# Kernel optimization log

Hardware: AMD Instinct MI355X
Metric: run time of the kernel (lower is better)

Reference implementation:

```python
import jax, jax.numpy as jnp
import numpy as np

EMD_DIM = 64
NB_EMD = 512


def setup_inputs() -> dict:
    key = jax.random.key(0)
    k_x, k_e = jax.random.split(key)
    x = jax.random.normal(k_x, (32, 64, 64, EMD_DIM), dtype=jnp.float32)
    # codebook buffer, shape [emd_dim, nb_emd] as in the torch module
    embed = jax.random.normal(k_e, (EMD_DIM, NB_EMD), dtype=jnp.float32)
    return {"x": x, "embed": embed}


def reference(x, embed):
    # Eval-mode forward (the EMA buffer update only runs under self.training
    # and does not affect this forward's outputs).
    flatten = x.reshape(-1, EMD_DIM)                      # [N, d]
    dist = (jnp.sum(flatten * flatten, axis=1, keepdims=True)
            - 2.0 * flatten @ embed
            + jnp.sum(embed * embed, axis=0, keepdims=True))  # [N, K]
    emd_id_flat = jnp.argmax(-dist, axis=1)               # nearest code index [N]
    emd_id = emd_id_flat.reshape(x.shape[:-1])            # [B, H, W]
    q = jnp.take(embed.T, emd_id, axis=0)                 # gather codes -> [B,H,W,d]
    diff = jnp.mean((jax.lax.stop_gradient(q) - x) ** 2)  # commitment loss
    q_st = x + jax.lax.stop_gradient(q - x)               # straight-through
    return (q_st, diff, emd_id)
```

## Files before the change

kernel.cpp:

```cpp
#include <hip/hip_runtime.h>

#define N_VEC 131072
#define D 64
#define K 512
#define GUARD 0.05f
#define NB_GATHER 2048
#define FB_Q 16

typedef __attribute__((ext_vector_type(8))) short bf16x8;
typedef __attribute__((ext_vector_type(4))) float f32x4;

static __device__ __forceinline__ short f2bf(float f) {
  unsigned u = __builtin_bit_cast(unsigned, f);
  u += 0x7fffu + ((u >> 16) & 1u);
  return (short)(u >> 16);
}
static __device__ __forceinline__ float bf2f(short h) {
  unsigned u = ((unsigned)(unsigned short)h) << 16;
  return __builtin_bit_cast(float, u);
}
static __device__ __forceinline__ void split8(const float4 f0, const float4 f1,
                                              bf16x8& h, bf16x8& m) {
  const float v[8] = {f0.x, f0.y, f0.z, f0.w, f1.x, f1.y, f1.z, f1.w};
#pragma unroll
  for (int j = 0; j < 8; ++j) {
    const short hh = f2bf(v[j]);
    h[j] = hh;
    m[j] = f2bf(v[j] - bf2f(hh));
  }
}

__global__ __launch_bounds__(64) void vq_prep_kernel(
    const float* __restrict__ embed, float* __restrict__ et,
    float* __restrict__ nrm, bf16x8* __restrict__ F, int* __restrict__ cnt)
{
  const int b = blockIdx.x;
  const int lane = threadIdx.x;
  if (b < 32) {
    const int row = lane & 15;
    const int kg  = lane >> 4;
    const int code = b * 16 + row;
#pragma unroll
    for (int c = 0; c < 2; ++c) {
      bf16x8 h, m;
#pragma unroll
      for (int j = 0; j < 8; ++j) {
        const int d = kg * 8 + c * 32 + j;
        const float e = embed[d * K + code];
        const short hh = f2bf(e);
        h[j] = hh;
        m[j] = f2bf(e - bf2f(hh));
      }
      F[b * 256 + c * 128 + 0  + lane] = h;
      F[b * 256 + c * 128 + 64 + lane] = m;
    }
  } else {
    if (b == 32 && lane == 0) cnt[0] = 0;
    const int code = (b - 32) * 64 + lane;
    float s = 0.f;
#pragma unroll
    for (int d = 0; d < D; ++d) {
      const float e = embed[d * K + code];
      et[code * D + d] = e;
      s = fmaf(e, e, s);
    }
    nrm[code] = s;
  }
}

__global__ __launch_bounds__(256, 4) void vq_coarse_kernel(
    const float* __restrict__ x, const bf16x8* __restrict__ F,
    const float* __restrict__ nrm, float* __restrict__ idf,
    int* __restrict__ cnt, int* __restrict__ list)
{
  const int tid  = threadIdx.x;
  const int lane = tid & 63;
  const int wid  = blockIdx.x * 4 + (tid >> 6);
  const int qbase = wid * 32;
  const int row = lane & 15;
  const int kg  = lane >> 4;

  bf16x8 Ah0c0, Ah0c1, Ah1c0, Ah1c1, Am0c0, Am0c1, Am1c0, Am1c1;
  {
    const float* xr0 = x + (size_t)(qbase + row) * D + kg * 8;
    const float* xr1 = x + (size_t)(qbase + 16 + row) * D + kg * 8;
    split8(*reinterpret_cast<const float4*>(xr0),
           *reinterpret_cast<const float4*>(xr0 + 4), Ah0c0, Am0c0);
    split8(*reinterpret_cast<const float4*>(xr0 + 32),
           *reinterpret_cast<const float4*>(xr0 + 36), Ah0c1, Am0c1);
    split8(*reinterpret_cast<const float4*>(xr1),
           *reinterpret_cast<const float4*>(xr1 + 4), Ah1c0, Am1c0);
    split8(*reinterpret_cast<const float4*>(xr1 + 32),
           *reinterpret_cast<const float4*>(xr1 + 36), Ah1c1, Am1c1);
  }

  float b1[8], b2[8]; int i1[8];
#pragma unroll
  for (int r = 0; r < 8; ++r) { b1[r] = 3.4e38f; b2[r] = 3.4e38f; i1[r] = 0; }

  bf16x8 Bh0 = F[lane], Bm0 = F[64 + lane], Bh1 = F[128 + lane], Bm1 = F[192 + lane];
  float nv = nrm[row];

#pragma unroll 1
  for (int t = 0; t < 32; ++t) {
    const int tn = (t + 1) & 31;
    const bf16x8 nBh0 = F[tn * 256 + lane];
    const bf16x8 nBm0 = F[tn * 256 + 64 + lane];
    const bf16x8 nBh1 = F[tn * 256 + 128 + lane];
    const bf16x8 nBm1 = F[tn * 256 + 192 + lane];
    const float nvn = nrm[tn * 16 + row];

    f32x4 a0 = {0.f, 0.f, 0.f, 0.f}, a1 = {0.f, 0.f, 0.f, 0.f};
    a0 = __builtin_amdgcn_mfma_f32_16x16x32_bf16(Ah0c0, Bh0, a0, 0, 0, 0);
    a1 = __builtin_amdgcn_mfma_f32_16x16x32_bf16(Ah1c0, Bh0, a1, 0, 0, 0);
    a0 = __builtin_amdgcn_mfma_f32_16x16x32_bf16(Ah0c1, Bh1, a0, 0, 0, 0);
    a1 = __builtin_amdgcn_mfma_f32_16x16x32_bf16(Ah1c1, Bh1, a1, 0, 0, 0);
    a0 = __builtin_amdgcn_mfma_f32_16x16x32_bf16(Ah0c0, Bm0, a0, 0, 0, 0);
    a1 = __builtin_amdgcn_mfma_f32_16x16x32_bf16(Ah1c0, Bm0, a1, 0, 0, 0);
    a0 = __builtin_amdgcn_mfma_f32_16x16x32_bf16(Ah0c1, Bm1, a0, 0, 0, 0);
    a1 = __builtin_amdgcn_mfma_f32_16x16x32_bf16(Ah1c1, Bm1, a1, 0, 0, 0);
    a0 = __builtin_amdgcn_mfma_f32_16x16x32_bf16(Am0c0, Bh0, a0, 0, 0, 0);
    a1 = __builtin_amdgcn_mfma_f32_16x16x32_bf16(Am1c0, Bh0, a1, 0, 0, 0);
    a0 = __builtin_amdgcn_mfma_f32_16x16x32_bf16(Am0c1, Bh1, a0, 0, 0, 0);
    a1 = __builtin_amdgcn_mfma_f32_16x16x32_bf16(Am1c1, Bh1, a1, 0, 0, 0);

    const int code = t * 16 + row;
#pragma unroll
    for (int r = 0; r < 4; ++r) {
      const float s0 = fmaf(-2.f, a0[r], nv);
      b2[r] = fminf(b2[r], fmaxf(b1[r], s0));
      if (s0 < b1[r]) { b1[r] = s0; i1[r] = code; }
      const float s1 = fmaf(-2.f, a1[r], nv);
      b2[4 + r] = fminf(b2[4 + r], fmaxf(b1[4 + r], s1));
      if (s1 < b1[4 + r]) { b1[4 + r] = s1; i1[4 + r] = code; }
    }
    Bh0 = nBh0; Bm0 = nBm0; Bh1 = nBh1; Bm1 = nBm1; nv = nvn;
  }

#pragma unroll
  for (int m = 1; m < 16; m <<= 1) {
#pragma unroll
    for (int r = 0; r < 8; ++r) {
      const float o1 = __shfl_xor(b1[r], m, 64);
      const int   oi = __shfl_xor(i1[r], m, 64);
      const float o2 = __shfl_xor(b2[r], m, 64);
      if (o1 < b1[r]) { b2[r] = fminf(b1[r], o2); b1[r] = o1; i1[r] = oi; }
      else            { b2[r] = fminf(b2[r], o1); }
    }
  }

  unsigned m32 = 0;
  if (row == 0) {
#pragma unroll
    for (int r = 0; r < 8; ++r) {
      const int qoff = (r >> 2) * 16 + kg * 4 + (r & 3);
      idf[qbase + qoff] = (float)i1[r];
      if (b2[r] - b1[r] < GUARD) m32 |= 1u << qoff;
    }
  }
  m32 |= __shfl_xor((int)m32, 16, 64);
  m32 |= __shfl_xor((int)m32, 32, 64);
  if (lane == 0 && m32) {
    int base = atomicAdd(cnt, __popc(m32));
    while (m32) {
      const int b = __ffs(m32) - 1;
      m32 &= m32 - 1;
      list[base++] = qbase + b;
    }
  }
}

__global__ __launch_bounds__(256) void vq_fallback_kernel(
    const float* __restrict__ x, const float* __restrict__ embed,
    const float* __restrict__ nrm, const int* __restrict__ cnt,
    const int* __restrict__ list, float* __restrict__ idf)
{
  __shared__ float x_lds[FB_Q * D];
  __shared__ int   s_qidx[FB_Q];
  __shared__ float s_best[4][FB_Q];
  __shared__ int   s_bid[4][FB_Q];
  const int tid  = threadIdx.x;
  const int lane = tid & 63;
  const int wv   = tid >> 6;
  const int n = cnt[0];

  for (int qb = blockIdx.x * FB_Q; qb < n; qb += gridDim.x * FB_Q) {
    __syncthreads();
    if (tid < FB_Q) {
      const int idx = qb + tid;
      s_qidx[tid] = list[idx < n ? idx : qb];
    }
    __syncthreads();
    {
      const int qj = tid >> 4, dq = tid & 15;
      *reinterpret_cast<float4*>(&x_lds[qj * D + dq * 4]) =
          *reinterpret_cast<const float4*>(x + (size_t)s_qidx[qj] * D + dq * 4);
    }
    __syncthreads();

    const int c0 = wv * 128 + lane;
    const int c1 = c0 + 64;
    float a0[FB_Q], a1[FB_Q];
#pragma unroll
    for (int i = 0; i < FB_Q; ++i) { a0[i] = 0.f; a1[i] = 0.f; }

#pragma unroll 4
    for (int ch = 0; ch < 16; ++ch) {
      const int d0 = ch * 4;
      const float e00 = embed[(d0 + 0) * K + c0];
      const float e01 = embed[(d0 + 0) * K + c1];
      const float e10 = embed[(d0 + 1) * K + c0];
      const float e11 = embed[(d0 + 1) * K + c1];
      const float e20 = embed[(d0 + 2) * K + c0];
      const float e21 = embed[(d0 + 2) * K + c1];
      const float e30 = embed[(d0 + 3) * K + c0];
      const float e31 = embed[(d0 + 3) * K + c1];
#pragma unroll
      for (int i = 0; i < FB_Q; ++i) {
        const float4 xv = *reinterpret_cast<const float4*>(&x_lds[i * D + d0]);
        a0[i] = fmaf(xv.x, e00, a0[i]);
        a0[i] = fmaf(xv.y, e10, a0[i]);
        a0[i] = fmaf(xv.z, e20, a0[i]);
        a0[i] = fmaf(xv.w, e30, a0[i]);
        a1[i] = fmaf(xv.x, e01, a1[i]);
        a1[i] = fmaf(xv.y, e11, a1[i]);
        a1[i] = fmaf(xv.z, e21, a1[i]);
        a1[i] = fmaf(xv.w, e31, a1[i]);
      }
    }

    const float nr0 = nrm[c0], nr1 = nrm[c1];
#pragma unroll
    for (int i = 0; i < FB_Q; ++i) {
      float best; int bid;
      const float s0 = fmaf(-2.f, a0[i], nr0);
      best = s0; bid = c0;
      const float s1 = fmaf(-2.f, a1[i], nr1);
      if (s1 < best) { best = s1; bid = c1; }
#pragma unroll
      for (int off = 32; off > 0; off >>= 1) {
        const float s2 = __shfl_down(best, off, 64);
        const int   b2 = __shfl_down(bid, off, 64);
        if (s2 < best || (s2 == best && b2 < bid)) { best = s2; bid = b2; }
      }
      if (lane == 0) { s_best[wv][i] = best; s_bid[wv][i] = bid; }
    }
    __syncthreads();
    if (tid < FB_Q) {
      float best = s_best[0][tid]; int bid = s_bid[0][tid];
#pragma unroll
      for (int w = 1; w < 4; ++w) {
        const float s = s_best[w][tid];
        if (s < best) { best = s; bid = s_bid[w][tid]; }
      }
      idf[s_qidx[tid]] = (float)bid;
    }
  }
}

__global__ __launch_bounds__(256) void vq_gather_kernel(
    const float* __restrict__ x, const float* __restrict__ et,
    const float* __restrict__ idf, float* __restrict__ q,
    float* __restrict__ partial)
{
  const int tid = blockIdx.x * 256 + threadIdx.x;
  const int stride = gridDim.x * 256;
  float acc = 0.f;
  for (int idx = tid; idx < N_VEC * (D / 4); idx += stride) {
    const int v = idx >> 4;
    const int d4 = idx & 15;
    const int id = (int)idf[v];
    const float4 xv = reinterpret_cast<const float4*>(x)[idx];
    const float4 ev = reinterpret_cast<const float4*>(et)[(id << 4) + d4];
    const float e0 = ev.x - xv.x, e1 = ev.y - xv.y, e2 = ev.z - xv.z, e3 = ev.w - xv.w;
    acc += (e0 * e0 + e1 * e1) + (e2 * e2 + e3 * e3);
    reinterpret_cast<float4*>(q)[idx] = ev;
  }
  acc += __shfl_down(acc, 32, 64);
  acc += __shfl_down(acc, 16, 64);
  acc += __shfl_down(acc, 8, 64);
  acc += __shfl_down(acc, 4, 64);
  acc += __shfl_down(acc, 2, 64);
  acc += __shfl_down(acc, 1, 64);
  __shared__ float sred[4];
  if ((threadIdx.x & 63) == 0) sred[threadIdx.x >> 6] = acc;
  __syncthreads();
  if (threadIdx.x == 0)
    partial[blockIdx.x] = (sred[0] + sred[1]) + (sred[2] + sred[3]);
}

__global__ __launch_bounds__(256) void vq_finalize_kernel(
    const float* __restrict__ partial, float* __restrict__ out)
{
  float acc = 0.f;
  for (int i = threadIdx.x; i < NB_GATHER; i += 256) acc += partial[i];
  acc += __shfl_down(acc, 32, 64);
  acc += __shfl_down(acc, 16, 64);
  acc += __shfl_down(acc, 8, 64);
  acc += __shfl_down(acc, 4, 64);
  acc += __shfl_down(acc, 2, 64);
  acc += __shfl_down(acc, 1, 64);
  __shared__ float sred[4];
  if ((threadIdx.x & 63) == 0) sred[threadIdx.x >> 6] = acc;
  __syncthreads();
  if (threadIdx.x == 0)
    out[0] = ((sred[0] + sred[1]) + (sred[2] + sred[3])) * (1.0f / (float)(N_VEC * D));
}

extern "C" void kernel_launch(void* const* d_in, const int* in_sizes, int n_in,
                              void* d_out, int out_size, void* d_ws, size_t ws_size,
                              hipStream_t stream) {
  const float* x = (const float*)d_in[0];
  const float* embed = (const float*)d_in[1];
  float* out = (float*)d_out;
  float* q    = out;
  float* diff = out + 8388608;
  float* idf  = out + 8388609;

  float* ws = (float*)d_ws;
  float* et      = ws;
  float* nrm     = ws + 32768;
  float* partial = ws + 33280;
  int*   cnt     = (int*)(ws + 35328);
  int*   list    = (int*)(ws + 35336);
  bf16x8* F = (bf16x8*)(ws + 35336 + N_VEC);

  vq_prep_kernel<<<40, 64, 0, stream>>>(embed, et, nrm, F, cnt);
  vq_coarse_kernel<<<N_VEC / 128, 256, 0, stream>>>(x, F, nrm, idf, cnt, list);
  vq_fallback_kernel<<<1024, 256, 0, stream>>>(x, embed, nrm, cnt, list, idf);
  vq_gather_kernel<<<NB_GATHER, 256, 0, stream>>>(x, et, idf, q, partial);
  vq_finalize_kernel<<<1, 256, 0, stream>>>(partial, diff);
}
```

Before: 86.50 us.

## Stage codebook tiles through double-buffered LDS and use med3 for second-best

Instead of each wavefront loading the full bf16 codebook tile from global memory every iteration, the four waves in a block now cooperatively load one tile into a double-buffered shared-memory array and read it from LDS. The goal is to cut redundant global/L2 traffic by a factor of four. The price is a block-wide barrier on every iteration and an extra LDS round trip. Separately, the second-best distance update is collapsed from a min/max pair into a single fmed3 instruction.

```diff
diff --git a/kernel.cpp b/kernel.cpp
--- a/kernel.cpp
+++ b/kernel.cpp
@@ -73,6 +73,7 @@
     const float* __restrict__ nrm, float* __restrict__ idf,
     int* __restrict__ cnt, int* __restrict__ list)
 {
+  __shared__ bf16x8 lb[2][256];
   const int tid  = threadIdx.x;
   const int lane = tid & 63;
   const int wid  = blockIdx.x * 4 + (tid >> 6);
@@ -98,17 +99,25 @@
 #pragma unroll
   for (int r = 0; r < 8; ++r) { b1[r] = 3.4e38f; b2[r] = 3.4e38f; i1[r] = 0; }
 
-  bf16x8 Bh0 = F[lane], Bm0 = F[64 + lane], Bh1 = F[128 + lane], Bm1 = F[192 + lane];
+  reinterpret_cast<float4*>(lb[0])[tid] = reinterpret_cast<const float4*>(F)[tid];
+  const float4* fs = reinterpret_cast<const float4*>(F) + 256 + tid;
+  const float* np = nrm + 16 + row;
   float nv = nrm[row];
+  __syncthreads();
 
 #pragma unroll 1
   for (int t = 0; t < 32; ++t) {
-    const int tn = (t + 1) & 31;
-    const bf16x8 nBh0 = F[tn * 256 + lane];
-    const bf16x8 nBm0 = F[tn * 256 + 64 + lane];
-    const bf16x8 nBh1 = F[tn * 256 + 128 + lane];
-    const bf16x8 nBm1 = F[tn * 256 + 192 + lane];
-    const float nvn = nrm[tn * 16 + row];
+    float4 f4; float nvn;
+    if (t < 31) {
+      f4 = *fs; fs += 256;
+      nvn = *np; np += 16;
+    }
+
+    const bf16x8* lbc = lb[t & 1];
+    const bf16x8 Bh0 = lbc[lane];
+    const bf16x8 Bm0 = lbc[64 + lane];
+    const bf16x8 Bh1 = lbc[128 + lane];
+    const bf16x8 Bm1 = lbc[192 + lane];
 
     f32x4 a0 = {0.f, 0.f, 0.f, 0.f}, a1 = {0.f, 0.f, 0.f, 0.f};
     a0 = __builtin_amdgcn_mfma_f32_16x16x32_bf16(Ah0c0, Bh0, a0, 0, 0, 0);
@@ -128,13 +137,18 @@
 #pragma unroll
     for (int r = 0; r < 4; ++r) {
       const float s0 = fmaf(-2.f, a0[r], nv);
-      b2[r] = fminf(b2[r], fmaxf(b1[r], s0));
+      b2[r] = __builtin_amdgcn_fmed3f(s0, b1[r], b2[r]);
       if (s0 < b1[r]) { b1[r] = s0; i1[r] = code; }
       const float s1 = fmaf(-2.f, a1[r], nv);
-      b2[4 + r] = fminf(b2[4 + r], fmaxf(b1[4 + r], s1));
+      b2[4 + r] = __builtin_amdgcn_fmed3f(s1, b1[4 + r], b2[4 + r]);
       if (s1 < b1[4 + r]) { b1[4 + r] = s1; i1[4 + r] = code; }
     }
-    Bh0 = nBh0; Bm0 = nBm0; Bh1 = nBh1; Bm1 = nBm1; nv = nvn;
+
+    if (t < 31) {
+      reinterpret_cast<float4*>(lb[(t + 1) & 1])[tid] = f4;
+      nv = nvn;
+    }
+    __syncthreads();
   }
 
 #pragma unroll
```

After: 84.31 us. 2.5% less time.
